# Performance work log

Measured on AMD Instinct MI355X. Metric: run time of the kernel, lower is better.

Reference implementation:

```python
import jax, jax.numpy as jnp
import numpy as np

BATCH, LEN, DIM = 8, 4096, 512


def setup_inputs() -> dict:
    key = jax.random.key(0)
    k1, k2, k3, k4, k5 = jax.random.split(key, 5)
    x = jax.random.normal(k1, (BATCH, LEN, DIM), dtype=jnp.float32)
    hidden_real = jax.random.normal(k2, (BATCH, DIM), dtype=jnp.float32)
    hidden_imag = jax.random.normal(k3, (BATCH, DIM), dtype=jnp.float32)
    phazor_init = jax.random.normal(k4, (DIM, 2), dtype=jnp.float32)
    phazor_param = jax.random.normal(k5, (DIM, 2), dtype=jnp.float32)
    return {
        "x": x,
        "hidden_real": hidden_real,
        "hidden_imag": hidden_imag,
        "phazor_init": phazor_init,
        "phazor_param": phazor_param,
    }


def _forward(x, hidden, phazor_init, phazor_param):
    L = x.shape[1]
    # view_as_complex of the (dim, 2) real params
    pz = phazor_param[:, 0] + 1j * phazor_param[:, 1]           # [dim] complex
    pi = phazor_init[:, 0] + 1j * phazor_init[:, 1]             # [dim] complex
    # phazor = exp(-|z|^2) * exp(i * angle(z))
    phazor = jnp.exp(-(pz.real * pz.real + pz.imag * pz.imag)) * jnp.exp(1j * jnp.angle(pz))
    # phazor^t for t = 0..L-1  -> [L, dim]
    prog = jnp.power(phazor[None, :], jnp.arange(L, dtype=jnp.float32)[:, None])
    filt = prog * pi[None, :]                                   # [L, dim]
    filt_fft = jnp.fft.fft(filt, n=2 * L, axis=0)               # [2L, dim]
    x_fft = jnp.fft.fft(x.astype(jnp.complex64), n=2 * L, axis=1)  # [B, 2L, dim]
    conv = jnp.fft.ifft(filt_fft[None, :, :] * x_fft, axis=1)[:, :L, :]  # [B, L, dim]
    conv_with_past = conv + hidden[:, None, :] * prog[None, :, :] * phazor[None, None, :]
    return conv_with_past.real, conv_with_past


def reference(x, hidden_real, hidden_imag, phazor_init, phazor_param):
    hidden = hidden_real + 1j * hidden_imag
    out_real, out_complex = _forward(x, hidden, phazor_init, phazor_param)
    return out_real, out_complex
```

## Files before the change

### kernel.cpp

```cpp
#include <hip/hip_runtime.h>
#include <math.h>

#define B 8
#define L 4096
#define D 512
#define LC 64
#define CK (L / LC)
#define BLD ((size_t)B * L * D)

typedef float v2f __attribute__((ext_vector_type(2)));

#define WS_PHZ   0
#define WS_PI    (2 * D)
#define WS_PTAB  (4 * D)
#define WS_LE    (4 * D + 2 * CK * D)
#define WS_FLOATS (WS_LE + 2 * B * CK * D)

__global__ __launch_bounds__(256) void setup_k(const float* __restrict__ pinit,
                                               const float* __restrict__ pparam,
                                               float* __restrict__ ws) {
    int idx = blockIdx.x * blockDim.x + threadIdx.x;
    if (idx >= CK * D) return;
    int d = idx % D;
    int c = idx / D;
    double a = (double)pparam[d * 2 + 0];
    double bb = (double)pparam[d * 2 + 1];
    double r2 = a * a + bb * bb;
    double inv = 1.0 / sqrt(r2);
    double mag = exp(-r2);
    double phr = mag * a * inv;
    double phi = mag * bb * inv;
    double rr = 1.0, ri = 0.0;
    double br = phr, bi = phi;
    int n = c * LC;
    while (n) {
        if (n & 1) {
            double tr = rr * br - ri * bi;
            double ti = rr * bi + ri * br;
            rr = tr; ri = ti;
        }
        double sr = br * br - bi * bi;
        double si = 2.0 * br * bi;
        br = sr; bi = si;
        n >>= 1;
    }
    ws[WS_PTAB + (c * D + d) * 2 + 0] = (float)rr;
    ws[WS_PTAB + (c * D + d) * 2 + 1] = (float)ri;
    if (c == 0) {
        ws[WS_PHZ + d * 2 + 0] = (float)phr;
        ws[WS_PHZ + d * 2 + 1] = (float)phi;
        ws[WS_PI + d * 2 + 0] = pinit[d * 2 + 0];
        ws[WS_PI + d * 2 + 1] = pinit[d * 2 + 1];
    }
}

__global__ __launch_bounds__(256) void pass1_k(const float* __restrict__ x,
                                               const float* __restrict__ ws,
                                               float* __restrict__ le) {
    int idx = blockIdx.x * blockDim.x + threadIdx.x;
    int d = idx % D;
    int c = (idx / D) % CK;
    int b = idx / (D * CK);
    v2f ph = *(const v2f*)(ws + WS_PHZ + d * 2);
    float ur = 0.f, ui = 0.f;
    const float* xp = x + ((size_t)b * L + (size_t)c * LC) * D + d;
#pragma unroll 8
    for (int i = 0; i < LC; ++i) {
        float xv = xp[(size_t)i * D];
        float nr = fmaf(ph.x, ur, fmaf(-ph.y, ui, xv));
        float ni = fmaf(ph.x, ui, ph.y * ur);
        ur = nr;
        ui = ni;
    }
    v2f lv; lv.x = ur; lv.y = ui;
    *(v2f*)(le + (size_t)idx * 2) = lv;
}

template <int MODE>
__global__ __launch_bounds__(256) void pass2_k(const float* __restrict__ x,
                                               const float* __restrict__ hr,
                                               const float* __restrict__ hi,
                                               const float* __restrict__ ws,
                                               const float* __restrict__ le,
                                               float* __restrict__ out) {
    int idx = blockIdx.x * blockDim.x + threadIdx.x;
    int d = idx % D;
    int c = (idx / D) % CK;
    int b = idx / (D * CK);

    v2f ph = *(const v2f*)(ws + WS_PHZ + d * 2);
    v2f q  = *(const v2f*)(ws + WS_PI + d * 2);
    const float* P = ws + WS_PTAB;

    float ur = 0.f, ui = 0.f;
    for (int j = 0; j < c; ++j) {
        int k = c - 1 - j;
        v2f Pk = *(const v2f*)(P + ((size_t)k * D + d) * 2);
        v2f lv = *(const v2f*)(le + (((size_t)b * CK + j) * D + d) * 2);
        ur = fmaf(Pk.x, lv.x, fmaf(-Pk.y, lv.y, ur));
        ui = fmaf(Pk.x, lv.y, fmaf(Pk.y, lv.x, ui));
    }

    v2f Pc = *(const v2f*)(P + ((size_t)c * D + d) * 2);
    float pwr = Pc.x * ph.x - Pc.y * ph.y;
    float pwi = fmaf(Pc.x, ph.y, Pc.y * ph.x);

    float hre = hr[(size_t)b * D + d];
    float him = hi[(size_t)b * D + d];

    const float* xp = x + ((size_t)b * L + (size_t)c * LC) * D + d;
    float* outr = out + ((size_t)b * L + (size_t)c * LC) * D + d;
    float* outr2 = outr + BLD;
    float* outc = out + BLD + (((size_t)b * L + (size_t)c * LC) * D + d) * 2;

#pragma unroll 4
    for (int i = 0; i < LC; ++i) {
        float xv = xp[(size_t)i * D];
        float nr = fmaf(ph.x, ur, fmaf(-ph.y, ui, xv));
        float ni = fmaf(ph.x, ui, ph.y * ur);
        ur = nr;
        ui = ni;
        float vr = fmaf(q.x, ur, fmaf(-q.y, ui, fmaf(hre, pwr, -him * pwi)));
        float vi = fmaf(q.x, ui, fmaf(q.y, ur, fmaf(hre, pwi, him * pwr)));
        outr[(size_t)i * D] = vr;
        if (MODE == 0) {
            outr2[(size_t)i * D] = vr;
        } else {
            v2f vc; vc.x = vr; vc.y = vi;
            *(v2f*)(outc + (size_t)i * D * 2) = vc;
        }
        float tr = fmaf(pwr, ph.x, -pwi * ph.y);
        float ti = fmaf(pwr, ph.y, pwi * ph.x);
        pwr = tr;
        pwi = ti;
    }
}

template <int MODE>
__global__ __launch_bounds__(256) void fallback_k(const float* __restrict__ x,
                                                  const float* __restrict__ hr,
                                                  const float* __restrict__ hi,
                                                  const float* __restrict__ pinit,
                                                  const float* __restrict__ pparam,
                                                  float* __restrict__ out) {
    int idx = blockIdx.x * blockDim.x + threadIdx.x;
    if (idx >= B * D) return;
    int d = idx % D;
    int b = idx / D;
    double a = (double)pparam[d * 2 + 0];
    double bb = (double)pparam[d * 2 + 1];
    double r2 = a * a + bb * bb;
    double inv = 1.0 / sqrt(r2);
    double mag = exp(-r2);
    float pr = (float)(mag * a * inv);
    float pim = (float)(mag * bb * inv);
    float qr = pinit[d * 2 + 0];
    float qi = pinit[d * 2 + 1];
    float hre = hr[(size_t)b * D + d];
    float him = hi[(size_t)b * D + d];
    float ur = 0.f, ui = 0.f;
    float pwr = pr, pwi = pim;
    const float* xp = x + (size_t)b * L * D + d;
    float* outr = out + (size_t)b * L * D + d;
    float* outr2 = outr + BLD;
    float* outc = out + BLD + ((size_t)b * L * D + d) * 2;
    for (int t = 0; t < L; ++t) {
        float xv = xp[(size_t)t * D];
        float nr = fmaf(pr, ur, fmaf(-pim, ui, xv));
        float ni = fmaf(pr, ui, pim * ur);
        ur = nr; ui = ni;
        float vr = fmaf(qr, ur, fmaf(-qi, ui, fmaf(hre, pwr, -him * pwi)));
        float vi = fmaf(qr, ui, fmaf(qi, ur, fmaf(hre, pwi, him * pwr)));
        outr[(size_t)t * D] = vr;
        if (MODE == 0) {
            outr2[(size_t)t * D] = vr;
        } else {
            v2f vc; vc.x = vr; vc.y = vi;
            *(v2f*)(outc + (size_t)t * D * 2) = vc;
        }
        float tr = fmaf(pwr, pr, -pwi * pim);
        float ti = fmaf(pwr, pim, pwi * pr);
        pwr = tr; pwi = ti;
    }
}

extern "C" void kernel_launch(void* const* d_in, const int* in_sizes, int n_in,
                              void* d_out, int out_size, void* d_ws, size_t ws_size,
                              hipStream_t stream) {
    const float* x = (const float*)d_in[0];
    const float* hreal = (const float*)d_in[1];
    const float* himag = (const float*)d_in[2];
    const float* pinit = (const float*)d_in[3];
    const float* pparam = (const float*)d_in[4];
    float* ws = (float*)d_ws;
    float* out = (float*)d_out;

    const int mode = (out_size >= (int)(3 * BLD)) ? 1 : 0;
    const bool fast = ws_size >= (size_t)WS_FLOATS * sizeof(float);

    if (fast) {
        float* le = ws + WS_LE;
        setup_k<<<(CK * D) / 256, 256, 0, stream>>>(pinit, pparam, ws);
        int n = B * CK * D;
        pass1_k<<<n / 256, 256, 0, stream>>>(x, ws, le);
        if (mode == 0)
            pass2_k<0><<<n / 256, 256, 0, stream>>>(x, hreal, himag, ws, le, out);
        else
            pass2_k<1><<<n / 256, 256, 0, stream>>>(x, hreal, himag, ws, le, out);
    } else {
        int n = B * D;
        if (mode == 0)
            fallback_k<0><<<(n + 255) / 256, 256, 0, stream>>>(x, hreal, himag, pinit, pparam, out);
        else
            fallback_k<1><<<(n + 255) / 256, 256, 0, stream>>>(x, hreal, himag, pinit, pparam, out);
    }
}
```

Before: 58.51 us.

## Drop setup kernel; compute phazor and chunk powers inline in float

Removes the separate double-precision setup kernel and its power table. Each thread now computes the phazor in float with rsqrt plus a Newton step and fast exp. It forms phazor^64 by repeated squaring and combines earlier chunk sums with a Horner-style recurrence instead of table lookups. This saves one kernel launch and the table traffic, at the cost of reduced precision in the powers, since float squaring replaces double binary exponentiation.

```diff
diff --git a/kernel.cpp b/kernel.cpp
--- a/kernel.cpp
+++ b/kernel.cpp
@@ -10,58 +10,27 @@
 
 typedef float v2f __attribute__((ext_vector_type(2)));
 
-#define WS_PHZ   0
-#define WS_PI    (2 * D)
-#define WS_PTAB  (4 * D)
-#define WS_LE    (4 * D + 2 * CK * D)
-#define WS_FLOATS (WS_LE + 2 * B * CK * D)
-
-__global__ __launch_bounds__(256) void setup_k(const float* __restrict__ pinit,
+#define WS_FLOATS (2 * B * CK * D)
+
+__device__ __forceinline__ v2f phazor_of(const float* __restrict__ pparam, int d) {
+    float a = pparam[d * 2 + 0];
+    float bb = pparam[d * 2 + 1];
+    float r2 = fmaf(a, a, bb * bb);
+    float inv = rsqrtf(r2);
+    inv = inv * fmaf(-0.5f * r2 * inv, inv, 1.5f);
+    float mag = __expf(-r2);
+    v2f p; p.x = mag * a * inv; p.y = mag * bb * inv;
+    return p;
+}
+
+__global__ __launch_bounds__(256) void pass1_k(const float* __restrict__ x,
                                                const float* __restrict__ pparam,
-                                               float* __restrict__ ws) {
-    int idx = blockIdx.x * blockDim.x + threadIdx.x;
-    if (idx >= CK * D) return;
-    int d = idx % D;
-    int c = idx / D;
-    double a = (double)pparam[d * 2 + 0];
-    double bb = (double)pparam[d * 2 + 1];
-    double r2 = a * a + bb * bb;
-    double inv = 1.0 / sqrt(r2);
-    double mag = exp(-r2);
-    double phr = mag * a * inv;
-    double phi = mag * bb * inv;
-    double rr = 1.0, ri = 0.0;
-    double br = phr, bi = phi;
-    int n = c * LC;
-    while (n) {
-        if (n & 1) {
-            double tr = rr * br - ri * bi;
-            double ti = rr * bi + ri * br;
-            rr = tr; ri = ti;
-        }
-        double sr = br * br - bi * bi;
-        double si = 2.0 * br * bi;
-        br = sr; bi = si;
-        n >>= 1;
-    }
-    ws[WS_PTAB + (c * D + d) * 2 + 0] = (float)rr;
-    ws[WS_PTAB + (c * D + d) * 2 + 1] = (float)ri;
-    if (c == 0) {
-        ws[WS_PHZ + d * 2 + 0] = (float)phr;
-        ws[WS_PHZ + d * 2 + 1] = (float)phi;
-        ws[WS_PI + d * 2 + 0] = pinit[d * 2 + 0];
-        ws[WS_PI + d * 2 + 1] = pinit[d * 2 + 1];
-    }
-}
-
-__global__ __launch_bounds__(256) void pass1_k(const float* __restrict__ x,
-                                               const float* __restrict__ ws,
                                                float* __restrict__ le) {
     int idx = blockIdx.x * blockDim.x + threadIdx.x;
     int d = idx % D;
     int c = (idx / D) % CK;
     int b = idx / (D * CK);
-    v2f ph = *(const v2f*)(ws + WS_PHZ + d * 2);
+    v2f ph = phazor_of(pparam, d);
     float ur = 0.f, ui = 0.f;
     const float* xp = x + ((size_t)b * L + (size_t)c * LC) * D + d;
 #pragma unroll 8
@@ -80,7 +49,8 @@
 __global__ __launch_bounds__(256) void pass2_k(const float* __restrict__ x,
                                                const float* __restrict__ hr,
                                                const float* __restrict__ hi,
-                                               const float* __restrict__ ws,
+                                               const float* __restrict__ pinit,
+                                               const float* __restrict__ pparam,
                                                const float* __restrict__ le,
                                                float* __restrict__ out) {
     int idx = blockIdx.x * blockDim.x + threadIdx.x;
@@ -88,22 +58,43 @@
     int c = (idx / D) % CK;
     int b = idx / (D * CK);
 
-    v2f ph = *(const v2f*)(ws + WS_PHZ + d * 2);
-    v2f q  = *(const v2f*)(ws + WS_PI + d * 2);
-    const float* P = ws + WS_PTAB;
+    v2f ph = phazor_of(pparam, d);
+    v2f q;  q.x = pinit[d * 2 + 0]; q.y = pinit[d * 2 + 1];
+
+    float br = ph.x, bi = ph.y;
+#pragma unroll
+    for (int s = 0; s < 6; ++s) {
+        float sr = fmaf(br, br, -bi * bi);
+        float si = 2.f * br * bi;
+        br = sr; bi = si;
+    }
 
     float ur = 0.f, ui = 0.f;
+    const float* lp = le + (((size_t)b * CK) * D + d) * 2;
     for (int j = 0; j < c; ++j) {
-        int k = c - 1 - j;
-        v2f Pk = *(const v2f*)(P + ((size_t)k * D + d) * 2);
-        v2f lv = *(const v2f*)(le + (((size_t)b * CK + j) * D + d) * 2);
-        ur = fmaf(Pk.x, lv.x, fmaf(-Pk.y, lv.y, ur));
-        ui = fmaf(Pk.x, lv.y, fmaf(Pk.y, lv.x, ui));
-    }
-
-    v2f Pc = *(const v2f*)(P + ((size_t)c * D + d) * 2);
-    float pwr = Pc.x * ph.x - Pc.y * ph.y;
-    float pwi = fmaf(Pc.x, ph.y, Pc.y * ph.x);
+        v2f lv = *(const v2f*)(lp + (size_t)j * D * 2);
+        float wr = fmaf(ur, br, fmaf(-ui, bi, lv.x));
+        float wi = fmaf(ur, bi, fmaf(ui, br, lv.y));
+        ur = wr; ui = wi;
+    }
+
+    float pwr = ph.x, pwi = ph.y;
+    {
+        float er = br, ei = bi;
+        int n = c;
+#pragma unroll
+        for (int s = 0; s < 6; ++s) {
+            if (n & 1) {
+                float tr = fmaf(pwr, er, -pwi * ei);
+                float ti = fmaf(pwr, ei, pwi * er);
+                pwr = tr; pwi = ti;
+            }
+            float sr = fmaf(er, er, -ei * ei);
+            float si = 2.f * er * ei;
+            er = sr; ei = si;
+            n >>= 1;
+        }
+    }
 
     float hre = hr[(size_t)b * D + d];
     float him = hi[(size_t)b * D + d];
@@ -147,27 +138,21 @@
     if (idx >= B * D) return;
     int d = idx % D;
     int b = idx / D;
-    double a = (double)pparam[d * 2 + 0];
-    double bb = (double)pparam[d * 2 + 1];
-    double r2 = a * a + bb * bb;
-    double inv = 1.0 / sqrt(r2);
-    double mag = exp(-r2);
-    float pr = (float)(mag * a * inv);
-    float pim = (float)(mag * bb * inv);
+    v2f ph = phazor_of(pparam, d);
     float qr = pinit[d * 2 + 0];
     float qi = pinit[d * 2 + 1];
     float hre = hr[(size_t)b * D + d];
     float him = hi[(size_t)b * D + d];
     float ur = 0.f, ui = 0.f;
-    float pwr = pr, pwi = pim;
+    float pwr = ph.x, pwi = ph.y;
     const float* xp = x + (size_t)b * L * D + d;
     float* outr = out + (size_t)b * L * D + d;
     float* outr2 = outr + BLD;
     float* outc = out + BLD + ((size_t)b * L * D + d) * 2;
     for (int t = 0; t < L; ++t) {
         float xv = xp[(size_t)t * D];
-        float nr = fmaf(pr, ur, fmaf(-pim, ui, xv));
-        float ni = fmaf(pr, ui, pim * ur);
+        float nr = fmaf(ph.x, ur, fmaf(-ph.y, ui, xv));
+        float ni = fmaf(ph.x, ui, ph.y * ur);
         ur = nr; ui = ni;
         float vr = fmaf(qr, ur, fmaf(-qi, ui, fmaf(hre, pwr, -him * pwi)));
         float vi = fmaf(qr, ui, fmaf(qi, ur, fmaf(hre, pwi, him * pwr)));
@@ -178,8 +163,8 @@
             v2f vc; vc.x = vr; vc.y = vi;
             *(v2f*)(outc + (size_t)t * D * 2) = vc;
         }
-        float tr = fmaf(pwr, pr, -pwi * pim);
-        float ti = fmaf(pwr, pim, pwi * pr);
+        float tr = fmaf(pwr, ph.x, -pwi * ph.y);
+        float ti = fmaf(pwr, ph.y, pwi * ph.x);
         pwr = tr; pwi = ti;
     }
 }
@@ -192,21 +177,19 @@
     const float* himag = (const float*)d_in[2];
     const float* pinit = (const float*)d_in[3];
     const float* pparam = (const float*)d_in[4];
-    float* ws = (float*)d_ws;
+    float* le = (float*)d_ws;
     float* out = (float*)d_out;
 
     const int mode = (out_size >= (int)(3 * BLD)) ? 1 : 0;
     const bool fast = ws_size >= (size_t)WS_FLOATS * sizeof(float);
 
     if (fast) {
-        float* le = ws + WS_LE;
-        setup_k<<<(CK * D) / 256, 256, 0, stream>>>(pinit, pparam, ws);
         int n = B * CK * D;
-        pass1_k<<<n / 256, 256, 0, stream>>>(x, ws, le);
+        pass1_k<<<n / 256, 256, 0, stream>>>(x, pparam, le);
         if (mode == 0)
-            pass2_k<0><<<n / 256, 256, 0, stream>>>(x, hreal, himag, ws, le, out);
+            pass2_k<0><<<n / 256, 256, 0, stream>>>(x, hreal, himag, pinit, pparam, le, out);
         else
-            pass2_k<1><<<n / 256, 256, 0, stream>>>(x, hreal, himag, ws, le, out);
+            pass2_k<1><<<n / 256, 256, 0, stream>>>(x, hreal, himag, pinit, pparam, le, out);
     } else {
         int n = B * D;
         if (mode == 0)
```

Measured after the change: 54.09 us. -7.6%, faster.
